# Kernel tuning notes

Hardware: AMD Instinct MI355X
Metric: run time of the kernel (lower is better)

Reference implementation:

```python
import jax, jax.numpy as jnp
import numpy as np

EMBED_DIM = 1024
NUM_HEADS = 16
HEAD_DIM = EMBED_DIM // NUM_HEADS


def setup_inputs() -> dict:
    key = jax.random.key(0)
    k1, k2, k3 = jax.random.split(key, 3)
    B, S = 2, 2048
    scale_in = 1.0 / np.sqrt(EMBED_DIM)
    x = jax.random.normal(k1, (B, S, EMBED_DIM), dtype=jnp.float32)
    Wqkv = jax.random.normal(k2, (EMBED_DIM, 3 * EMBED_DIM), dtype=jnp.float32) * scale_in
    bqkv = jnp.zeros((3 * EMBED_DIM,), dtype=jnp.float32)
    Wout = jax.random.normal(k3, (EMBED_DIM, EMBED_DIM), dtype=jnp.float32) * scale_in
    bout = jnp.zeros((EMBED_DIM,), dtype=jnp.float32)
    return {"x": x, "Wqkv": Wqkv, "bqkv": bqkv, "Wout": Wout, "bout": bout}


def reference(x, Wqkv, bqkv, Wout, bout):
    # Causal multi-head self-attention (dropout in eval mode = identity).
    B, S, E = x.shape
    qkv = x @ Wqkv + bqkv                                  # [B,S,3E]
    qkv = qkv.reshape(B, S, 3, NUM_HEADS, HEAD_DIM)
    qkv = jnp.transpose(qkv, (2, 0, 3, 1, 4))              # [3,B,H,S,D]
    q, k, v = qkv[0], qkv[1], qkv[2]
    scores = jnp.einsum("bhqd,bhkd->bhqk", q, k) / np.sqrt(HEAD_DIM)
    causal = jnp.tril(jnp.ones((S, S), dtype=bool))
    scores = jnp.where(causal, scores, -jnp.inf)
    attn = jax.nn.softmax(scores, axis=-1)                 # [B,H,S,S]
    out = jnp.einsum("bhqk,bhkd->bhqd", attn, v)           # [B,H,S,D]
    out = jnp.transpose(out, (0, 2, 1, 3)).reshape(B, S, E)
    return out @ Wout + bout
```

## Files before the change

### kernel.cpp

```cpp
#include <hip/hip_runtime.h>
#include <hip/hip_bf16.h>

#define BB 2
#define SS 2048
#define EE 1024
#define HH 16
#define DD 64
#define MT (BB*SS)
#define NQ (3*EE)

typedef unsigned short u16;
typedef __bf16 bf16t;
typedef bf16t bf16x8 __attribute__((ext_vector_type(8)));
typedef short short8v __attribute__((ext_vector_type(8)));
typedef float f32x4 __attribute__((ext_vector_type(4)));

#define AS1 __attribute__((address_space(1)))
#define AS3 __attribute__((address_space(3)))

__device__ __forceinline__ u16 f2b(float f) {
  unsigned u = __builtin_bit_cast(unsigned, f);
  u += 0x7FFF + ((u >> 16) & 1);
  return (u16)(u >> 16);
}

__device__ __forceinline__ unsigned cvtpk(float lo, float hi) {
  unsigned r;
  asm("v_cvt_pk_bf16_f32 %0, %1, %2" : "=v"(r) : "v"(lo), "v"(hi));
  return r;
}

__device__ __forceinline__ void gload_lds16(const void* g, void* l) {
  __builtin_amdgcn_global_load_lds((const AS1 void*)(g), (AS3 void*)(l), 16, 0, 0);
}

__device__ __forceinline__ f32x4 mfma_bf16(short8v a, short8v b, f32x4 c) {
  return __builtin_amdgcn_mfma_f32_16x16x32_bf16(
      __builtin_bit_cast(bf16x8, a), __builtin_bit_cast(bf16x8, b), c, 0, 0, 0);
}

#define QSCALE 0.18033688f

__global__ void __launch_bounds__(256) cast_kernel(const float* __restrict__ in,
                                                   u16* __restrict__ out, int n) {
  int i = (blockIdx.x * 256 + threadIdx.x) * 4;
  if (i + 3 < n) {
    float4 v = *(const float4*)(in + i);
    ushort4 o;
    o.x = f2b(v.x); o.y = f2b(v.y); o.z = f2b(v.z); o.w = f2b(v.w);
    *(ushort4*)(out + i) = o;
  }
}

__global__ void __launch_bounds__(256) transpose_kernel(const float* __restrict__ W,
                                                        u16* __restrict__ WT,
                                                        int K, int N) {
  __shared__ float t[64][65];
  int k0 = blockIdx.y * 64, n0 = blockIdx.x * 64;
  int r = threadIdx.x >> 4;
  int c4 = (threadIdx.x & 15) * 4;
#pragma unroll
  for (int i = 0; i < 4; ++i) {
    float4 v = *(const float4*)(W + (size_t)(k0 + r + i * 16) * N + n0 + c4);
    t[r + i * 16][c4 + 0] = v.x; t[r + i * 16][c4 + 1] = v.y;
    t[r + i * 16][c4 + 2] = v.z; t[r + i * 16][c4 + 3] = v.w;
  }
  __syncthreads();
#pragma unroll
  for (int i = 0; i < 4; ++i) {
    ushort4 o;
    o.x = f2b(t[c4 + 0][r + i * 16]); o.y = f2b(t[c4 + 1][r + i * 16]);
    o.z = f2b(t[c4 + 2][r + i * 16]); o.w = f2b(t[c4 + 3][r + i * 16]);
    *(ushort4*)(WT + (size_t)(n0 + r + i * 16) * K + k0 + c4) = o;
  }
}

__global__ void __launch_bounds__(256) gemm_qkv_kernel(
    const u16* __restrict__ A, const u16* __restrict__ BT,
    const float* __restrict__ bias,
    u16* __restrict__ Qs, u16* __restrict__ Ks, u16* __restrict__ Vt) {
  __shared__ u16 As[4096];
  __shared__ u16 Bs[4096];
  const int K = EE;
  int tid = threadIdx.x;
  int w = tid >> 6, lane = tid & 63;
  int g = lane >> 4, q = lane & 15;
  int m0 = blockIdx.y * 128, n0 = blockIdx.x * 128;
  int wm = (w >> 1) * 64, wn = (w & 1) * 64;

  f32x4 acc[4][4] = {};

  int r = tid >> 2;
  int kc = (tid & 3) * 8;
  const u16* ga = A + (size_t)(m0 + r) * K + kc;
  const u16* gb = BT + (size_t)(n0 + r) * K + kc;
  u16* lA0 = As + w * 512;
  u16* lA1 = As + 2048 + w * 512;
  u16* lB0 = Bs + w * 512;
  u16* lB1 = Bs + 2048 + w * 512;

  for (int k0 = 0; k0 < K; k0 += 32) {
    gload_lds16(ga, lA0);
    gload_lds16(ga + 64 * K, lA1);
    gload_lds16(gb, lB0);
    gload_lds16(gb + 64 * K, lB1);
    ga += 32; gb += 32;
    __syncthreads();
    short8v af[4], bfv[4];
#pragma unroll
    for (int m = 0; m < 4; ++m)
      af[m] = *(const short8v*)(As + (wm + m * 16 + q) * 32 + g * 8);
#pragma unroll
    for (int n = 0; n < 4; ++n)
      bfv[n] = *(const short8v*)(Bs + (wn + n * 16 + q) * 32 + g * 8);
#pragma unroll
    for (int m = 0; m < 4; ++m)
#pragma unroll
      for (int n = 0; n < 4; ++n)
        acc[m][n] = mfma_bf16(af[m], bfv[n], acc[m][n]);
    __syncthreads();
  }

#pragma unroll
  for (int m = 0; m < 4; ++m) {
    int row0 = m0 + wm + m * 16 + g * 4;
#pragma unroll
    for (int n = 0; n < 4; ++n) {
      int col = n0 + wn + n * 16 + q;
      float bi = bias[col];
      int t = col >> 10;
      int h = (col >> 6) & 15;
      int d = col & 63;
      int b = row0 >> 11, s0 = row0 & 2047;
      size_t bh = (size_t)b * HH + h;
      if (t == 2) {
        ushort4 vv;
        vv.x = f2b(acc[m][n][0] + bi); vv.y = f2b(acc[m][n][1] + bi);
        vv.z = f2b(acc[m][n][2] + bi); vv.w = f2b(acc[m][n][3] + bi);
        *(ushort4*)&Vt[(bh * DD + d) * SS + s0] = vv;
      } else if (t == 0) {
#pragma unroll
        for (int r2 = 0; r2 < 4; ++r2)
          Qs[(bh * SS + s0 + r2) * DD + d] = f2b((acc[m][n][r2] + bi) * QSCALE);
      } else {
#pragma unroll
        for (int r2 = 0; r2 < 4; ++r2)
          Ks[(bh * SS + s0 + r2) * DD + d] = f2b(acc[m][n][r2] + bi);
      }
    }
  }
}

__global__ void __launch_bounds__(512) attn_kernel(
    const u16* __restrict__ Qg, const u16* __restrict__ Kg,
    const u16* __restrict__ Vg, u16* __restrict__ O) {
  __shared__ char lds[49152];
  const int tid = threadIdx.x;
  const int w = tid >> 6, lane = tid & 63;
  const int g = lane >> 4, q = lane & 15;
  const int bid = blockIdx.x;
  const int bh = bid & 31;
  const int p = 15 - (bid >> 5);
  const int b = bh >> 4, h = bh & 15;
  char* Pw = lds + 32768 + w * 2048;
  const int qsw = (q & 7) << 4;

  const char* Qp = (const char*)Qg + (size_t)bh * (SS * 128);
  const char* Kp = (const char*)Kg + (size_t)bh * (SS * 128);
  const char* Vp = (const char*)Vg + (size_t)bh * (SS * 128);

  const int srow = tid >> 3;
  const int ssw = ((tid & 7) * 16) ^ ((srow & 7) << 4);
  const char* Ksrc = Kp + srow * 128 + ssw;
  const char* Vsrc = Vp + (size_t)srow * (SS * 2) + ssw;
  char* Kdst = lds + w * 1024;
  char* Vdst = lds + 16384 + w * 1024;

  const int nt = 2 * p + 2;
  const int qw = p * 128 + w * 16;

  short8v aq0 = *(const short8v*)(Qp + (size_t)(qw + q) * 128 + g * 16);
  short8v aq1 = *(const short8v*)(Qp + (size_t)(qw + q) * 128 + 64 + g * 16);

  f32x4 oacc[4] = {};
  float mrun = -1e30f, lrun = 0.f;

  gload_lds16(Ksrc, Kdst);
  gload_lds16(Vsrc, Vdst);
  __syncthreads();

  for (int s = 0; s < nt; ++s) {
    const int buf = s & 1;
    if (s + 1 < nt) {
      gload_lds16(Ksrc + (size_t)(s + 1) * 8192, Kdst + (buf ^ 1) * 8192);
      gload_lds16(Vsrc + (s + 1) * 128, Vdst + (buf ^ 1) * 8192);
    }
    const int kv0 = s << 6;
    if (kv0 <= qw + 15) {
      const char* Kc = lds + buf * 8192;
      const char* Vc = lds + 16384 + buf * 8192;
      short8v kf[4][2];
#pragma unroll
      for (int cc = 0; cc < 4; ++cc) {
        const char* kb = Kc + (cc * 16 + q) * 128;
        kf[cc][0] = *(const short8v*)(kb + ((g * 16) ^ qsw));
        kf[cc][1] = *(const short8v*)(kb + ((64 + g * 16) ^ qsw));
      }
      f32x4 st[4];
#pragma unroll
      for (int cc = 0; cc < 4; ++cc) {
        f32x4 z = {};
        z = mfma_bf16(kf[cc][0], aq0, z);
        z = mfma_bf16(kf[cc][1], aq1, z);
        st[cc] = z;
      }
      short8v vf[4][2];
#pragma unroll
      for (int v = 0; v < 4; ++v) {
        const char* vb = Vc + (v * 16 + q) * 128;
        vf[v][0] = *(const short8v*)(vb + ((g * 16) ^ qsw));
        vf[v][1] = *(const short8v*)(vb + ((64 + g * 16) ^ qsw));
      }
      if (kv0 + 63 > qw) {
        int row = qw + q;
#pragma unroll
        for (int cc = 0; cc < 4; ++cc) {
          int kvb = kv0 + cc * 16 + g * 4;
#pragma unroll
          for (int r2 = 0; r2 < 4; ++r2)
            if (kvb + r2 > row) st[cc][r2] = -1e30f;
        }
      }
      f32x4 t01, t23;
#pragma unroll
      for (int r2 = 0; r2 < 4; ++r2) {
        t01[r2] = fmaxf(st[0][r2], st[1][r2]);
        t23[r2] = fmaxf(st[2][r2], st[3][r2]);
      }
      float mx = fmaxf(fmaxf(fmaxf(t01[0], t01[1]), fmaxf(t01[2], t01[3])),
                       fmaxf(fmaxf(t23[0], t23[1]), fmaxf(t23[2], t23[3])));
      mx = fmaxf(mx, __shfl_xor(mx, 16));
      mx = fmaxf(mx, __shfl_xor(mx, 32));
      if (!__all(mx - mrun <= 8.f)) {
        float mnew = fmaxf(mrun, mx);
        float alpha = exp2f(mrun - mnew);
        mrun = mnew;
        lrun *= alpha;
#pragma unroll
        for (int vfi = 0; vfi < 4; ++vfi)
#pragma unroll
          for (int r2 = 0; r2 < 4; ++r2) oacc[vfi][r2] *= alpha;
      }
      f32x4 sum4 = {};
#pragma unroll
      for (int cc = 0; cc < 4; ++cc)
#pragma unroll
        for (int r2 = 0; r2 < 4; ++r2) {
          float pv = exp2f(st[cc][r2] - mrun);
          st[cc][r2] = pv;
          sum4[r2] += pv;
        }
      float sm = (sum4[0] + sum4[1]) + (sum4[2] + sum4[3]);
      sm += __shfl_xor(sm, 16);
      sm += __shfl_xor(sm, 32);
      lrun += sm;
      char* basep = Pw + q * 128;
#pragma unroll
      for (int cc = 0; cc < 4; ++cc) {
        unsigned p01 = cvtpk(st[cc][0], st[cc][1]);
        unsigned p23 = cvtpk(st[cc][2], st[cc][3]);
        *(unsigned*)(basep + ((32 * cc + 8 * g + 0) ^ qsw)) = p01;
        *(unsigned*)(basep + ((32 * cc + 8 * g + 4) ^ qsw)) = p23;
      }
      short8v pa0 = *(const short8v*)(basep + ((g * 16) ^ qsw));
      short8v pa1 = *(const short8v*)(basep + ((64 + g * 16) ^ qsw));
#pragma unroll
      for (int vfi = 0; vfi < 4; ++vfi) {
        oacc[vfi] = mfma_bf16(vf[vfi][0], pa0, oacc[vfi]);
        oacc[vfi] = mfma_bf16(vf[vfi][1], pa1, oacc[vfi]);
      }
    }
    __syncthreads();
  }

  {
    float inv = 1.0f / lrun;
    int row = qw + q;
    char* obase = (char*)O + (((size_t)b * SS + row) * EE + h * 64) * 2;
#pragma unroll
    for (int vfi = 0; vfi < 4; ++vfi) {
      uint2 o;
      o.x = cvtpk(oacc[vfi][0] * inv, oacc[vfi][1] * inv);
      o.y = cvtpk(oacc[vfi][2] * inv, oacc[vfi][3] * inv);
      *(uint2*)(obase + (vfi * 16 + g * 4) * 2) = o;
    }
  }
}

__global__ void __launch_bounds__(256) gemm_out_kernel(
    const u16* __restrict__ A, const u16* __restrict__ BT,
    const float* __restrict__ bias, float* __restrict__ Cout) {
  __shared__ u16 As[4096];
  __shared__ u16 Bs[4096];
  const int K = EE;
  int tid = threadIdx.x;
  int w = tid >> 6, lane = tid & 63;
  int g = lane >> 4, q = lane & 15;
  int m0 = blockIdx.y * 128, n0 = blockIdx.x * 128;
  int wm = (w >> 1) * 64, wn = (w & 1) * 64;

  f32x4 acc[4][4] = {};

  int r = tid >> 2;
  int kc = (tid & 3) * 8;
  const u16* ga = A + (size_t)(m0 + r) * K + kc;
  const u16* gb = BT + (size_t)(n0 + r) * K + kc;
  u16* lA0 = As + w * 512;
  u16* lA1 = As + 2048 + w * 512;
  u16* lB0 = Bs + w * 512;
  u16* lB1 = Bs + 2048 + w * 512;

  for (int k0 = 0; k0 < K; k0 += 32) {
    gload_lds16(ga, lA0);
    gload_lds16(ga + 64 * K, lA1);
    gload_lds16(gb, lB0);
    gload_lds16(gb + 64 * K, lB1);
    ga += 32; gb += 32;
    __syncthreads();
    short8v af[4], bfv[4];
#pragma unroll
    for (int m = 0; m < 4; ++m)
      af[m] = *(const short8v*)(As + (wm + m * 16 + q) * 32 + g * 8);
#pragma unroll
    for (int n = 0; n < 4; ++n)
      bfv[n] = *(const short8v*)(Bs + (wn + n * 16 + q) * 32 + g * 8);
#pragma unroll
    for (int m = 0; m < 4; ++m)
#pragma unroll
      for (int n = 0; n < 4; ++n)
        acc[m][n] = mfma_bf16(af[m], bfv[n], acc[m][n]);
    __syncthreads();
  }

#pragma unroll
  for (int m = 0; m < 4; ++m) {
    int row0 = m0 + wm + m * 16 + g * 4;
#pragma unroll
    for (int n = 0; n < 4; ++n) {
      int col = n0 + wn + n * 16 + q;
      float bi = bias[col];
#pragma unroll
      for (int r2 = 0; r2 < 4; ++r2) {
        int row = row0 + r2;
        Cout[(size_t)row * EE + col] = acc[m][n][r2] + bi;
      }
    }
  }
}

extern "C" void kernel_launch(void* const* d_in, const int* in_sizes, int n_in,
                              void* d_out, int out_size, void* d_ws, size_t ws_size,
                              hipStream_t stream) {
  (void)in_sizes; (void)n_in; (void)out_size; (void)ws_size;
  const float* x    = (const float*)d_in[0];
  const float* Wqkv = (const float*)d_in[1];
  const float* bqkv = (const float*)d_in[2];
  const float* Wout = (const float*)d_in[3];
  const float* bout = (const float*)d_in[4];
  float* out = (float*)d_out;

  char* p = (char*)d_ws;
  u16* xb  = (u16*)p; p += (size_t)MT * EE * 2;
  u16* wqT = (u16*)p; p += (size_t)NQ * EE * 2;
  u16* woT = (u16*)p; p += (size_t)EE * EE * 2;
  u16* Qs  = (u16*)p; p += (size_t)BB * HH * SS * DD * 2;
  u16* Ks  = (u16*)p; p += (size_t)BB * HH * SS * DD * 2;
  u16* Vt  = (u16*)p; p += (size_t)BB * HH * DD * SS * 2;
  u16* Ob  = (u16*)p; p += (size_t)MT * EE * 2;

  cast_kernel<<<dim3((MT * EE / 4) / 256), dim3(256), 0, stream>>>(x, xb, MT * EE);
  transpose_kernel<<<dim3(NQ / 64, EE / 64), dim3(256), 0, stream>>>(Wqkv, wqT, EE, NQ);
  transpose_kernel<<<dim3(EE / 64, EE / 64), dim3(256), 0, stream>>>(Wout, woT, EE, EE);
  gemm_qkv_kernel<<<dim3(NQ / 128, MT / 128), dim3(256), 0, stream>>>(xb, wqT, bqkv, Qs, Ks, Vt);
  attn_kernel<<<dim3(512), dim3(512), 0, stream>>>(Qs, Ks, Vt, Ob);
  gemm_out_kernel<<<dim3(EE / 128, MT / 128), dim3(256), 0, stream>>>(Ob, woT, bout, out);
}
```

Before: 137.3 us.

## Double-buffer LDS tiles in QKV and output projection GEMMs

Both projection GEMMs now hold two LDS buffers per operand. The first K-tile is prefetched before the loop, and each iteration issues the global-to-LDS loads for the next tile before computing on the current one. This cuts the loop to one barrier per iteration and lets global memory latency overlap with the MFMA work. In exchange, shared memory per block doubles, which could lower occupancy.

```diff
diff --git a/kernel.cpp b/kernel.cpp
--- a/kernel.cpp
+++ b/kernel.cpp
@@ -79,8 +79,8 @@
     const u16* __restrict__ A, const u16* __restrict__ BT,
     const float* __restrict__ bias,
     u16* __restrict__ Qs, u16* __restrict__ Ks, u16* __restrict__ Vt) {
-  __shared__ u16 As[4096];
-  __shared__ u16 Bs[4096];
+  __shared__ u16 As[8192];
+  __shared__ u16 Bs[8192];
   const int K = EE;
   int tid = threadIdx.x;
   int w = tid >> 6, lane = tid & 63;
@@ -99,26 +99,39 @@
   u16* lB0 = Bs + w * 512;
   u16* lB1 = Bs + 2048 + w * 512;
 
+  gload_lds16(ga, lA0);
+  gload_lds16(ga + 64 * K, lA1);
+  gload_lds16(gb, lB0);
+  gload_lds16(gb + 64 * K, lB1);
+  ga += 32; gb += 32;
+  __syncthreads();
+
+  int cur = 0;
   for (int k0 = 0; k0 < K; k0 += 32) {
-    gload_lds16(ga, lA0);
-    gload_lds16(ga + 64 * K, lA1);
-    gload_lds16(gb, lB0);
-    gload_lds16(gb + 64 * K, lB1);
-    ga += 32; gb += 32;
-    __syncthreads();
+    if (k0 + 32 < K) {
+      int nx = (cur ^ 1) * 4096;
+      gload_lds16(ga, lA0 + nx);
+      gload_lds16(ga + 64 * K, lA1 + nx);
+      gload_lds16(gb, lB0 + nx);
+      gload_lds16(gb + 64 * K, lB1 + nx);
+      ga += 32; gb += 32;
+    }
+    const u16* Ab = As + cur * 4096;
+    const u16* Bb = Bs + cur * 4096;
     short8v af[4], bfv[4];
 #pragma unroll
     for (int m = 0; m < 4; ++m)
-      af[m] = *(const short8v*)(As + (wm + m * 16 + q) * 32 + g * 8);
+      af[m] = *(const short8v*)(Ab + (wm + m * 16 + q) * 32 + g * 8);
 #pragma unroll
     for (int n = 0; n < 4; ++n)
-      bfv[n] = *(const short8v*)(Bs + (wn + n * 16 + q) * 32 + g * 8);
+      bfv[n] = *(const short8v*)(Bb + (wn + n * 16 + q) * 32 + g * 8);
 #pragma unroll
     for (int m = 0; m < 4; ++m)
 #pragma unroll
       for (int n = 0; n < 4; ++n)
         acc[m][n] = mfma_bf16(af[m], bfv[n], acc[m][n]);
     __syncthreads();
+    cur ^= 1;
   }
 
 #pragma unroll
@@ -300,8 +313,8 @@
 __global__ void __launch_bounds__(256) gemm_out_kernel(
     const u16* __restrict__ A, const u16* __restrict__ BT,
     const float* __restrict__ bias, float* __restrict__ Cout) {
-  __shared__ u16 As[4096];
-  __shared__ u16 Bs[4096];
+  __shared__ u16 As[8192];
+  __shared__ u16 Bs[8192];
   const int K = EE;
   int tid = threadIdx.x;
   int w = tid >> 6, lane = tid & 63;
@@ -320,26 +333,39 @@
   u16* lB0 = Bs + w * 512;
   u16* lB1 = Bs + 2048 + w * 512;
 
+  gload_lds16(ga, lA0);
+  gload_lds16(ga + 64 * K, lA1);
+  gload_lds16(gb, lB0);
+  gload_lds16(gb + 64 * K, lB1);
+  ga += 32; gb += 32;
+  __syncthreads();
+
+  int cur = 0;
   for (int k0 = 0; k0 < K; k0 += 32) {
-    gload_lds16(ga, lA0);
-    gload_lds16(ga + 64 * K, lA1);
-    gload_lds16(gb, lB0);
-    gload_lds16(gb + 64 * K, lB1);
-    ga += 32; gb += 32;
-    __syncthreads();
+    if (k0 + 32 < K) {
+      int nx = (cur ^ 1) * 4096;
+      gload_lds16(ga, lA0 + nx);
+      gload_lds16(ga + 64 * K, lA1 + nx);
+      gload_lds16(gb, lB0 + nx);
+      gload_lds16(gb + 64 * K, lB1 + nx);
+      ga += 32; gb += 32;
+    }
+    const u16* Ab = As + cur * 4096;
+    const u16* Bb = Bs + cur * 4096;
     short8v af[4], bfv[4];
 #pragma unroll
     for (int m = 0; m < 4; ++m)
-      af[m] = *(const short8v*)(As + (wm + m * 16 + q) * 32 + g * 8);
+      af[m] = *(const short8v*)(Ab + (wm + m * 16 + q) * 32 + g * 8);
 #pragma unroll
     for (int n = 0; n < 4; ++n)
-      bfv[n] = *(const short8v*)(Bs + (wn + n * 16 + q) * 32 + g * 8);
+      bfv[n] = *(const short8v*)(Bb + (wn + n * 16 + q) * 32 + g * 8);
 #pragma unroll
     for (int m = 0; m < 4; ++m)
 #pragma unroll
       for (int n = 0; n < 4; ++n)
         acc[m][n] = mfma_bf16(af[m], bfv[n], acc[m][n]);
     __syncthreads();
+    cur ^= 1;
   }
 
 #pragma unroll
```

After: 121.1 us. 11.8% less time.
